# Performance work log

Measured on AMD Instinct MI355X. Metric: run time of the kernel, lower is better.

Reference implementation:

```python
import jax, jax.numpy as jnp
import numpy as np

B, O, D = 4096, 256, 256  # batch, size_out (rules), size_in (features)


def setup_inputs() -> dict:
    key = jax.random.key(0)
    k1, k2, k3, k4, k5 = jax.random.split(key, 5)
    return {
        "x": jax.random.normal(k1, (B, D), dtype=jnp.float32),
        "scales": jax.random.normal(k2, (O, D), dtype=jnp.float32),
        # strict upper triangle holds the packed rot vectors (original inits them to zeros;
        # small values keep the quadratic form well conditioned)
        "rots": jax.random.normal(k3, (O, D, D), dtype=jnp.float32) * 0.02,
        "centroids": jax.random.normal(k4, (O, D, 1), dtype=jnp.float32),
        "b": jax.random.uniform(k5, (O,), dtype=jnp.float32, minval=0.5, maxval=1.5),
    }


def reference(x, scales, rots, centroids, b):
    # Build symmetric transform A[o] = diag(scales[o]) + triu(rots[o],1) + triu(rots[o],1)^T
    # (equivalent to the loop of diag_embed(r_i, i+1) + mirrored lower diagonal).
    upper = jnp.triu(rots, 1)                                   # [O,D,D]
    A = upper + jnp.swapaxes(upper, -1, -2)
    A = A + jnp.eye(D, dtype=scales.dtype) * scales[:, None, :]  # diag_embed(scales)
    # Augmented affine map: mul[o,i,b'] = A[o] @ x[b'] + centroid[o,i]; const row dropped
    # since only the first size_in rows feed the norm.
    y = jnp.einsum('bj,oij->boi', x, A) + centroids[..., 0][None, :, :]  # [B,O,D]
    rx = jnp.sqrt(jnp.sum(y * y, axis=-1))                      # L2 norm over D -> [B,O]
    return 1.0 / (1.0 + rx ** (2.0 * b))                        # bell membership [B,O]
```

## Files before the change

kernel.cpp:

```cpp
#include <hip/hip_runtime.h>
#include <cstdint>
#include <cmath>

#define Bn 4096
#define Dn 256
#define On 256

typedef __bf16 v8bf __attribute__((ext_vector_type(8)));
typedef float  v4f  __attribute__((ext_vector_type(4)));
typedef unsigned short us8 __attribute__((ext_vector_type(8)));

__device__ __forceinline__ unsigned short f2bf(float f) {
    unsigned int u = __builtin_bit_cast(unsigned int, f);
    unsigned int r = (u + 0x7fffu + ((u >> 16) & 1u)) >> 16;
    return (unsigned short)r;
}

__device__ __forceinline__ void gl_lds16(const void* g, void* l) {
    __builtin_amdgcn_global_load_lds(
        (const __attribute__((address_space(1))) void*)(uintptr_t)g,
        (__attribute__((address_space(3))) void*)(uintptr_t)l, 16, 0, 0);
}

__global__ __launch_bounds__(256) void prep(
    const float* __restrict__ scales, const float* __restrict__ rots,
    const float* __restrict__ x, unsigned short* __restrict__ Ap,
    unsigned short* __restrict__ xb) {
    const int bid = blockIdx.x;
    const int tid = threadIdx.x;

    if (bid >= 2560) {
        const int cb = bid - 2560;
#pragma unroll
        for (int s = 0; s < 4; ++s) {
            const int i = cb * 4096 + s * 1024 + tid * 4;
            const float4 v = *(const float4*)(x + i);
            ushort4 u;
            u.x = f2bf(v.x); u.y = f2bf(v.y); u.z = f2bf(v.z); u.w = f2bf(v.w);
            *(ushort4*)(xb + i) = u;
        }
        return;
    }

    static const int TI[10] = {0, 0, 0, 0, 1, 1, 1, 2, 2, 3};
    static const int TJ[10] = {0, 1, 2, 3, 1, 2, 3, 2, 3, 3};
    const int o  = bid / 10;
    const int p  = bid - o * 10;
    const int ti = TI[p], tj = TJ[p];

    __shared__ float t[64][68];
    const float* src = rots + (size_t)o * Dn * Dn + (size_t)(ti * 64) * Dn + tj * 64;
#pragma unroll
    for (int s = 0; s < 4; ++s) {
        const int idx = s * 256 + tid;
        const int r = idx >> 4, c = (idx & 15) * 4;
        const float4 v = *(const float4*)(src + r * Dn + c);
        *(float4*)&t[r][c] = v;
    }
    __syncthreads();

#pragma unroll
    for (int it = 0; it < 2; ++it) {
        const int slot = it * 256 + tid;
        const int bk = slot >> 6, L = slot & 63;
        const int quad = L >> 4, frow = L & 15;
        const int sl = bk >> 1, kl = bk & 1;
        const int r = sl * 16 + frow, c = kl * 32 + quad * 8;
        float v[8];
        if (ti == tj) {
#pragma unroll
            for (int q = 0; q < 8; ++q) {
                const int cc = c + q;
                v[q] = (r < cc) ? t[r][cc]
                     : ((r > cc) ? t[cc][r] : scales[o * Dn + ti * 64 + r]);
            }
        } else {
            const float4 a = *(const float4*)&t[r][c];
            const float4 b = *(const float4*)&t[r][c + 4];
            v[0] = a.x; v[1] = a.y; v[2] = a.z; v[3] = a.w;
            v[4] = b.x; v[5] = b.y; v[6] = b.z; v[7] = b.w;
        }
        us8 u;
#pragma unroll
        for (int q = 0; q < 8; ++q) u[q] = f2bf(v[q]);
        const size_t off = ((size_t)((o * 16 + ti * 4 + sl) * 8 + tj * 2 + kl)) * 512 + L * 8;
        *(us8*)(Ap + off) = u;
    }

    if (ti != tj) {
#pragma unroll
        for (int it = 0; it < 2; ++it) {
            const int slot = it * 256 + tid;
            const int bk = slot >> 6, L = slot & 63;
            const int quad = L >> 4, frow = L & 15;
            const int sl = bk >> 1, kl = bk & 1;
            const int r = sl * 16 + frow, c = kl * 32 + quad * 8;
            us8 u;
#pragma unroll
            for (int q = 0; q < 8; ++q) u[q] = f2bf(t[c + q][r]);
            const size_t off = ((size_t)((o * 16 + tj * 4 + sl) * 8 + ti * 2 + kl)) * 512 + L * 8;
            *(us8*)(Ap + off) = u;
        }
    }
}

__global__ __launch_bounds__(256, 2) void fuzzy_main(
    const unsigned short* __restrict__ Ap, const unsigned short* __restrict__ xb,
    const float* __restrict__ cent, const float* __restrict__ bvals,
    float* __restrict__ obase, int sb, int so) {
    __shared__ __align__(16) unsigned short Xs[128 * 256];
    __shared__ float ssbuf[4][128];
    __shared__ float centL[Dn];

    const int tid  = threadIdx.x;
    const int lane = tid & 63;
    const int wv   = tid >> 6;
    const int Lb = blockIdx.x;
    const int o  = (Lb & 7) * 32 + (Lb >> 8);
    const int b0 = ((Lb >> 3) & 31) * 128;

    centL[tid] = cent[o * Dn + tid];

#pragma unroll
    for (int q = 0; q < 16; ++q) {
        const int R   = wv * 16 + q;
        const int row = 2 * R + (lane >> 5);
        const int g   = (lane & 31) ^ (row & 7);
        gl_lds16(xb + (size_t)(b0 + row) * Dn + g * 8, &Xs[R * 512 + lane * 8]);
    }
    __syncthreads();

    const int frow = lane & 15, quad = lane >> 4, f3 = lane & 7;
    const unsigned short* Aw = Ap + (size_t)(o * 16 + wv * 4) * 4096;

    v4f acc[4][8];
#pragma unroll
    for (int mi = 0; mi < 4; ++mi)
#pragma unroll
        for (int ni = 0; ni < 8; ++ni)
            acc[mi][ni] = v4f{0.f, 0.f, 0.f, 0.f};

    v8bf af[2][4];
#pragma unroll
    for (int mi = 0; mi < 4; ++mi)
        af[0][mi] = *(const v8bf*)(Aw + (size_t)mi * 8 * 512 + lane * 8);

#pragma unroll
    for (int t = 0; t < 8; ++t) {
        const int cur = t & 1, nxt = cur ^ 1;
        if (t < 7) {
#pragma unroll
            for (int mi = 0; mi < 4; ++mi)
                af[nxt][mi] = *(const v8bf*)(Aw + (size_t)(mi * 8 + t + 1) * 512 + lane * 8);
        }
        v8bf xf[8];
        const int sl = (t * 4 + quad) ^ f3;
#pragma unroll
        for (int ni = 0; ni < 8; ++ni)
            xf[ni] = *(const v8bf*)&Xs[(ni * 16 + frow) * 256 + sl * 8];
#pragma unroll
        for (int mi = 0; mi < 4; ++mi)
#pragma unroll
            for (int ni = 0; ni < 8; ++ni)
                acc[mi][ni] = __builtin_amdgcn_mfma_f32_16x16x32_bf16(
                    af[cur][mi], xf[ni], acc[mi][ni], 0, 0, 0);
    }

    float cv[4][4];
#pragma unroll
    for (int mi = 0; mi < 4; ++mi)
#pragma unroll
        for (int rg = 0; rg < 4; ++rg)
            cv[mi][rg] = centL[wv * 64 + mi * 16 + quad * 4 + rg];
#pragma unroll
    for (int ni = 0; ni < 8; ++ni) {
        float v = 0.f;
#pragma unroll
        for (int mi = 0; mi < 4; ++mi)
#pragma unroll
            for (int rg = 0; rg < 4; ++rg) {
                const float y = acc[mi][ni][rg] + cv[mi][rg];
                v += y * y;
            }
        v += __shfl_xor(v, 16);
        v += __shfl_xor(v, 32);
        if (lane < 16) ssbuf[wv][ni * 16 + lane] = v;
    }
    __syncthreads();
    if (tid < 128) {
        const float ssq = ssbuf[0][tid] + ssbuf[1][tid] + ssbuf[2][tid] + ssbuf[3][tid];
        obase[(size_t)(b0 + tid) * sb + (size_t)o * so] =
            1.0f / (1.0f + powf(ssq, bvals[o]));
    }
}

__global__ __launch_bounds__(256) void transp(const float* __restrict__ outT,
                                              float* __restrict__ out) {
    __shared__ float t[64][65];
    const int bb = blockIdx.x * 64;
    const int ob = blockIdx.y * 64;
    const int tid = threadIdx.x;
    const int r = tid >> 4;
    const int c = (tid & 15) * 4;
#pragma unroll
    for (int s = 0; s < 4; ++s) {
        const int rr = s * 16 + r;
        const float4 v = *(const float4*)(outT + (size_t)(ob + rr) * Bn + bb + c);
        t[rr][c] = v.x; t[rr][c + 1] = v.y; t[rr][c + 2] = v.z; t[rr][c + 3] = v.w;
    }
    __syncthreads();
#pragma unroll
    for (int s = 0; s < 4; ++s) {
        const int rr = s * 16 + r;
        float4 w;
        w.x = t[c][rr]; w.y = t[c + 1][rr]; w.z = t[c + 2][rr]; w.w = t[c + 3][rr];
        *(float4*)(out + (size_t)(bb + rr) * On + ob + c) = w;
    }
}

__global__ void fallback_kernel(const float* __restrict__ x, const float* __restrict__ scales,
                                const float* __restrict__ rots, const float* __restrict__ cent,
                                const float* __restrict__ bvals, float* __restrict__ out) {
    const int b = blockIdx.x * blockDim.x + threadIdx.x;
    const int o = blockIdx.y;
    if (b >= Bn) return;
    const float* R  = rots + (size_t)o * Dn * Dn;
    const float* xv = x + (size_t)b * Dn;
    float ss = 0.f;
    for (int i = 0; i < Dn; ++i) {
        float a = cent[o * Dn + i];
        for (int j = 0; j < Dn; ++j) {
            const float w = (j > i) ? R[i * Dn + j]
                          : ((j < i) ? R[j * Dn + i] : scales[o * Dn + i]);
            a += w * xv[j];
        }
        ss += a * a;
    }
    out[(size_t)b * On + o] = 1.f / (1.f + powf(ss, bvals[o]));
}

extern "C" void kernel_launch(void* const* d_in, const int* in_sizes, int n_in,
                              void* d_out, int out_size, void* d_ws, size_t ws_size,
                              hipStream_t stream) {
    const float* x         = (const float*)d_in[0];
    const float* scales    = (const float*)d_in[1];
    const float* rots      = (const float*)d_in[2];
    const float* centroids = (const float*)d_in[3];
    const float* bvals     = (const float*)d_in[4];
    float* out = (float*)d_out;

    const size_t needA = (size_t)On * Dn * Dn * sizeof(unsigned short);
    const size_t needX = (size_t)Bn * Dn * sizeof(unsigned short);
    const size_t needT = (size_t)On * Bn * sizeof(float);

    if (ws_size >= needA + needX) {
        unsigned short* Ap = (unsigned short*)d_ws;
        unsigned short* xb = (unsigned short*)((char*)d_ws + needA);
        prep<<<dim3(2816), 256, 0, stream>>>(scales, rots, x, Ap, xb);
        if (ws_size >= needA + needX + needT) {
            float* outT = (float*)((char*)d_ws + needA + needX);
            fuzzy_main<<<dim3(8192), 256, 0, stream>>>(Ap, xb, centroids, bvals,
                                                       outT, 1, Bn);
            transp<<<dim3(Bn / 64, On / 64), 256, 0, stream>>>(outT, out);
        } else {
            fuzzy_main<<<dim3(8192), 256, 0, stream>>>(Ap, xb, centroids, bvals,
                                                       out, On, 1);
        }
    } else {
        fallback_kernel<<<dim3(Bn / 256, On), 256, 0, stream>>>(x, scales, rots, centroids,
                                                                bvals, out);
    }
}
```

Baseline: 249.4 us.

## Process four rules per block to reuse X tile and drop transpose kernel

```diff
diff --git a/kernel.cpp b/kernel.cpp
--- a/kernel.cpp
+++ b/kernel.cpp
@@ -107,114 +107,105 @@
 __global__ __launch_bounds__(256, 2) void fuzzy_main(
     const unsigned short* __restrict__ Ap, const unsigned short* __restrict__ xb,
     const float* __restrict__ cent, const float* __restrict__ bvals,
-    float* __restrict__ obase, int sb, int so) {
-    __shared__ __align__(16) unsigned short Xs[128 * 256];
-    __shared__ float ssbuf[4][128];
-    __shared__ float centL[Dn];
+    float* __restrict__ out) {
+    __shared__ __align__(16) unsigned short Xs[4][128 * 64];
+    __shared__ float ssbufA[4][4][128];
+    __shared__ float centL[4][Dn];
 
     const int tid  = threadIdx.x;
     const int lane = tid & 63;
     const int wv   = tid >> 6;
     const int Lb = blockIdx.x;
-    const int o  = (Lb & 7) * 32 + (Lb >> 8);
+    const int og = (Lb & 7) * 8 + (Lb >> 8);
     const int b0 = ((Lb >> 3) & 31) * 128;
 
-    centL[tid] = cent[o * Dn + tid];
-
-#pragma unroll
-    for (int q = 0; q < 16; ++q) {
-        const int R   = wv * 16 + q;
-        const int row = 2 * R + (lane >> 5);
-        const int g   = (lane & 31) ^ (row & 7);
-        gl_lds16(xb + (size_t)(b0 + row) * Dn + g * 8, &Xs[R * 512 + lane * 8]);
-    }
+#pragma unroll
+    for (int op = 0; op < 4; ++op)
+        centL[op][tid] = cent[(og * 4 + op) * Dn + tid];
+
+    const int frow = lane & 15, quad = lane >> 4, f3 = lane & 7;
+    const int lr = lane >> 3, ls = lane & 7;
+    const int ksw = (ls ^ lr) * 8;
+
+#pragma unroll
+    for (int c = 0; c < 4; ++c)
+#pragma unroll
+        for (int q = 0; q < 4; ++q) {
+            const int row = (wv * 4 + q) * 8 + lr;
+            gl_lds16(xb + (size_t)(b0 + row) * Dn + c * 64 + ksw,
+                     &Xs[c][row * 64 + ls * 8]);
+        }
     __syncthreads();
 
-    const int frow = lane & 15, quad = lane >> 4, f3 = lane & 7;
-    const unsigned short* Aw = Ap + (size_t)(o * 16 + wv * 4) * 4096;
-
-    v4f acc[4][8];
-#pragma unroll
-    for (int mi = 0; mi < 4; ++mi)
-#pragma unroll
-        for (int ni = 0; ni < 8; ++ni)
-            acc[mi][ni] = v4f{0.f, 0.f, 0.f, 0.f};
-
-    v8bf af[2][4];
-#pragma unroll
-    for (int mi = 0; mi < 4; ++mi)
-        af[0][mi] = *(const v8bf*)(Aw + (size_t)mi * 8 * 512 + lane * 8);
-
-#pragma unroll
-    for (int t = 0; t < 8; ++t) {
-        const int cur = t & 1, nxt = cur ^ 1;
-        if (t < 7) {
+    for (int op = 0; op < 4; ++op) {
+        const int o = og * 4 + op;
+        const unsigned short* Aw = Ap + (size_t)(o * 16 + wv * 4) * 4096;
+
+        v4f acc[4][8];
+#pragma unroll
+        for (int mi = 0; mi < 4; ++mi)
+#pragma unroll
+            for (int ni = 0; ni < 8; ++ni)
+                acc[mi][ni] = v4f{0.f, 0.f, 0.f, 0.f};
+
+        v8bf af[2][4];
+#pragma unroll
+        for (int mi = 0; mi < 4; ++mi)
+            af[0][mi] = *(const v8bf*)(Aw + (size_t)mi * 8 * 512 + lane * 8);
+
+#pragma unroll
+        for (int t = 0; t < 8; ++t) {
+            const int cur = t & 1, nxt = cur ^ 1;
+            if (t < 7) {
+#pragma unroll
+                for (int mi = 0; mi < 4; ++mi)
+                    af[nxt][mi] = *(const v8bf*)(Aw + (size_t)(mi * 8 + t + 1) * 512 + lane * 8);
+            }
+            v8bf xf[8];
+            const int sl = ((t & 1) * 4 + quad) ^ f3;
+#pragma unroll
+            for (int ni = 0; ni < 8; ++ni)
+                xf[ni] = *(const v8bf*)&Xs[t >> 1][(ni * 16 + frow) * 64 + sl * 8];
 #pragma unroll
             for (int mi = 0; mi < 4; ++mi)
-                af[nxt][mi] = *(const v8bf*)(Aw + (size_t)(mi * 8 + t + 1) * 512 + lane * 8);
-        }
-        v8bf xf[8];
-        const int sl = (t * 4 + quad) ^ f3;
-#pragma unroll
-        for (int ni = 0; ni < 8; ++ni)
-            xf[ni] = *(const v8bf*)&Xs[(ni * 16 + frow) * 256 + sl * 8];
+#pragma unroll
+                for (int ni = 0; ni < 8; ++ni)
+                    acc[mi][ni] = __builtin_amdgcn_mfma_f32_16x16x32_bf16(
+                        af[cur][mi], xf[ni], acc[mi][ni], 0, 0, 0);
+        }
+
+        float cv[4][4];
 #pragma unroll
         for (int mi = 0; mi < 4; ++mi)
 #pragma unroll
-            for (int ni = 0; ni < 8; ++ni)
-                acc[mi][ni] = __builtin_amdgcn_mfma_f32_16x16x32_bf16(
-                    af[cur][mi], xf[ni], acc[mi][ni], 0, 0, 0);
-    }
-
-    float cv[4][4];
-#pragma unroll
-    for (int mi = 0; mi < 4; ++mi)
-#pragma unroll
-        for (int rg = 0; rg < 4; ++rg)
-            cv[mi][rg] = centL[wv * 64 + mi * 16 + quad * 4 + rg];
-#pragma unroll
-    for (int ni = 0; ni < 8; ++ni) {
-        float v = 0.f;
-#pragma unroll
-        for (int mi = 0; mi < 4; ++mi)
-#pragma unroll
-            for (int rg = 0; rg < 4; ++rg) {
-                const float y = acc[mi][ni][rg] + cv[mi][rg];
-                v += y * y;
-            }
-        v += __shfl_xor(v, 16);
-        v += __shfl_xor(v, 32);
-        if (lane < 16) ssbuf[wv][ni * 16 + lane] = v;
+            for (int rg = 0; rg < 4; ++rg)
+                cv[mi][rg] = centL[op][wv * 64 + mi * 16 + quad * 4 + rg];
+#pragma unroll
+        for (int ni = 0; ni < 8; ++ni) {
+            float v = 0.f;
+#pragma unroll
+            for (int mi = 0; mi < 4; ++mi)
+#pragma unroll
+                for (int rg = 0; rg < 4; ++rg) {
+                    const float y = acc[mi][ni][rg] + cv[mi][rg];
+                    v += y * y;
+                }
+            v += __shfl_xor(v, 16);
+            v += __shfl_xor(v, 32);
+            if (lane < 16) ssbufA[op][wv][ni * 16 + lane] = v;
+        }
     }
     __syncthreads();
     if (tid < 128) {
-        const float ssq = ssbuf[0][tid] + ssbuf[1][tid] + ssbuf[2][tid] + ssbuf[3][tid];
-        obase[(size_t)(b0 + tid) * sb + (size_t)o * so] =
-            1.0f / (1.0f + powf(ssq, bvals[o]));
-    }
-}
-
-__global__ __launch_bounds__(256) void transp(const float* __restrict__ outT,
-                                              float* __restrict__ out) {
-    __shared__ float t[64][65];
-    const int bb = blockIdx.x * 64;
-    const int ob = blockIdx.y * 64;
-    const int tid = threadIdx.x;
-    const int r = tid >> 4;
-    const int c = (tid & 15) * 4;
-#pragma unroll
-    for (int s = 0; s < 4; ++s) {
-        const int rr = s * 16 + r;
-        const float4 v = *(const float4*)(outT + (size_t)(ob + rr) * Bn + bb + c);
-        t[rr][c] = v.x; t[rr][c + 1] = v.y; t[rr][c + 2] = v.z; t[rr][c + 3] = v.w;
-    }
-    __syncthreads();
-#pragma unroll
-    for (int s = 0; s < 4; ++s) {
-        const int rr = s * 16 + r;
-        float4 w;
-        w.x = t[c][rr]; w.y = t[c + 1][rr]; w.z = t[c + 2][rr]; w.w = t[c + 3][rr];
-        *(float4*)(out + (size_t)(bb + rr) * On + ob + c) = w;
+        float4 r;
+        float* rp = &r.x;
+#pragma unroll
+        for (int op = 0; op < 4; ++op) {
+            const float ssq = ssbufA[op][0][tid] + ssbufA[op][1][tid] +
+                              ssbufA[op][2][tid] + ssbufA[op][3][tid];
+            rp[op] = 1.0f / (1.0f + powf(ssq, bvals[og * 4 + op]));
+        }
+        *(float4*)(out + (size_t)(b0 + tid) * On + og * 4) = r;
     }
 }
 
@@ -251,21 +242,12 @@
 
     const size_t needA = (size_t)On * Dn * Dn * sizeof(unsigned short);
     const size_t needX = (size_t)Bn * Dn * sizeof(unsigned short);
-    const size_t needT = (size_t)On * Bn * sizeof(float);
 
     if (ws_size >= needA + needX) {
         unsigned short* Ap = (unsigned short*)d_ws;
         unsigned short* xb = (unsigned short*)((char*)d_ws + needA);
         prep<<<dim3(2816), 256, 0, stream>>>(scales, rots, x, Ap, xb);
-        if (ws_size >= needA + needX + needT) {
-            float* outT = (float*)((char*)d_ws + needA + needX);
-            fuzzy_main<<<dim3(8192), 256, 0, stream>>>(Ap, xb, centroids, bvals,
-                                                       outT, 1, Bn);
-            transp<<<dim3(Bn / 64, On / 64), 256, 0, stream>>>(outT, out);
-        } else {
-            fuzzy_main<<<dim3(8192), 256, 0, stream>>>(Ap, xb, centroids, bvals,
-                                                       out, On, 1);
-        }
+        fuzzy_main<<<dim3(2048), 256, 0, stream>>>(Ap, xb, centroids, bvals, out);
     } else {
         fallback_kernel<<<dim3(Bn / 256, On), 256, 0, stream>>>(x, scales, rots, centroids,
                                                                 bvals, out);
```

After: 487.3 us. 1.95x slower.

## Switch main GEMM to 32x32x16 bf16 MFMA with matching operand layouts

Applied to the files above, without the earlier changes.

```diff
diff --git a/kernel.cpp b/kernel.cpp
--- a/kernel.cpp
+++ b/kernel.cpp
@@ -7,7 +7,7 @@
 #define On 256
 
 typedef __bf16 v8bf __attribute__((ext_vector_type(8)));
-typedef float  v4f  __attribute__((ext_vector_type(4)));
+typedef float  v16f __attribute__((ext_vector_type(16)));
 typedef unsigned short us8 __attribute__((ext_vector_type(8)));
 
 __device__ __forceinline__ unsigned short f2bf(float f) {
@@ -59,46 +59,43 @@
     }
     __syncthreads();
 
+    const int L   = tid & 63;
+    const int kl  = (tid >> 6) & 3;
+    const int i32 = L & 31;
+    const int kb  = kl * 16 + (L >> 5) * 8;
+
 #pragma unroll
     for (int it = 0; it < 2; ++it) {
-        const int slot = it * 256 + tid;
-        const int bk = slot >> 6, L = slot & 63;
-        const int quad = L >> 4, frow = L & 15;
-        const int sl = bk >> 1, kl = bk & 1;
-        const int r = sl * 16 + frow, c = kl * 32 + quad * 8;
+        const int r = it * 32 + i32;
         float v[8];
         if (ti == tj) {
 #pragma unroll
             for (int q = 0; q < 8; ++q) {
-                const int cc = c + q;
+                const int cc = kb + q;
                 v[q] = (r < cc) ? t[r][cc]
                      : ((r > cc) ? t[cc][r] : scales[o * Dn + ti * 64 + r]);
             }
         } else {
-            const float4 a = *(const float4*)&t[r][c];
-            const float4 b = *(const float4*)&t[r][c + 4];
+            const float4 a = *(const float4*)&t[r][kb];
+            const float4 b = *(const float4*)&t[r][kb + 4];
             v[0] = a.x; v[1] = a.y; v[2] = a.z; v[3] = a.w;
             v[4] = b.x; v[5] = b.y; v[6] = b.z; v[7] = b.w;
         }
         us8 u;
 #pragma unroll
         for (int q = 0; q < 8; ++q) u[q] = f2bf(v[q]);
-        const size_t off = ((size_t)((o * 16 + ti * 4 + sl) * 8 + tj * 2 + kl)) * 512 + L * 8;
+        const size_t off = ((size_t)((o * 8 + ti * 2 + it) * 16 + tj * 4 + kl)) * 512 + L * 8;
         *(us8*)(Ap + off) = u;
     }
 
     if (ti != tj) {
 #pragma unroll
         for (int it = 0; it < 2; ++it) {
-            const int slot = it * 256 + tid;
-            const int bk = slot >> 6, L = slot & 63;
-            const int quad = L >> 4, frow = L & 15;
-            const int sl = bk >> 1, kl = bk & 1;
-            const int r = sl * 16 + frow, c = kl * 32 + quad * 8;
+            const int r = it * 32 + i32;
             us8 u;
 #pragma unroll
-            for (int q = 0; q < 8; ++q) u[q] = f2bf(t[c + q][r]);
-            const size_t off = ((size_t)((o * 16 + tj * 4 + sl) * 8 + ti * 2 + kl)) * 512 + L * 8;
+            for (int q = 0; q < 8; ++q) u[q] = f2bf(t[kb + q][r]);
+            const size_t off = ((size_t)((o * 8 + tj * 2 + it) * 16 + ti * 4 + kl)) * 512 + L * 8;
             *(us8*)(Ap + off) = u;
         }
     }
@@ -108,7 +105,7 @@
     const unsigned short* __restrict__ Ap, const unsigned short* __restrict__ xb,
     const float* __restrict__ cent, const float* __restrict__ bvals,
     float* __restrict__ obase, int sb, int so) {
-    __shared__ __align__(16) unsigned short Xs[128 * 256];
+    __shared__ __align__(16) unsigned short Xs[64 * 512];
     __shared__ float ssbuf[4][128];
     __shared__ float centL[Dn];
 
@@ -123,68 +120,67 @@
 
 #pragma unroll
     for (int q = 0; q < 16; ++q) {
-        const int R   = wv * 16 + q;
-        const int row = 2 * R + (lane >> 5);
-        const int g   = (lane & 31) ^ (row & 7);
-        gl_lds16(xb + (size_t)(b0 + row) * Dn + g * 8, &Xs[R * 512 + lane * 8]);
-    }
-    __syncthreads();
-
-    const int frow = lane & 15, quad = lane >> 4, f3 = lane & 7;
-    const unsigned short* Aw = Ap + (size_t)(o * 16 + wv * 4) * 4096;
-
-    v4f acc[4][8];
-#pragma unroll
-    for (int mi = 0; mi < 4; ++mi)
-#pragma unroll
-        for (int ni = 0; ni < 8; ++ni)
-            acc[mi][ni] = v4f{0.f, 0.f, 0.f, 0.f};
-
-    v8bf af[2][4];
-#pragma unroll
-    for (int mi = 0; mi < 4; ++mi)
-        af[0][mi] = *(const v8bf*)(Aw + (size_t)mi * 8 * 512 + lane * 8);
-
-#pragma unroll
-    for (int t = 0; t < 8; ++t) {
+        const int R  = wv * 16 + q;
+        const int tt = R >> 2, nb = R & 3;
+        gl_lds16(xb + (size_t)(b0 + nb * 32 + (lane & 31)) * Dn + tt * 16 + (lane >> 5) * 8,
+                 &Xs[R * 512 + lane * 8]);
+    }
+
+    const unsigned short* Aw = Ap + (size_t)(o * 8 + wv * 2) * 16 * 512;
+
+    v16f acc[2][4];
+#pragma unroll
+    for (int mi = 0; mi < 2; ++mi)
+#pragma unroll
+        for (int nb = 0; nb < 4; ++nb)
+#pragma unroll
+            for (int rg = 0; rg < 16; ++rg)
+                acc[mi][nb][rg] = 0.f;
+
+    v8bf af[2][2], xf[2][4];
+#pragma unroll
+    for (int mi = 0; mi < 2; ++mi)
+        af[0][mi] = *(const v8bf*)(Aw + (size_t)(mi * 16) * 512 + lane * 8);
+
+    __syncthreads();
+
+#pragma unroll
+    for (int nb = 0; nb < 4; ++nb)
+        xf[0][nb] = *(const v8bf*)&Xs[nb * 512 + lane * 8];
+
+#pragma unroll
+    for (int t = 0; t < 16; ++t) {
         const int cur = t & 1, nxt = cur ^ 1;
-        if (t < 7) {
-#pragma unroll
-            for (int mi = 0; mi < 4; ++mi)
-                af[nxt][mi] = *(const v8bf*)(Aw + (size_t)(mi * 8 + t + 1) * 512 + lane * 8);
-        }
-        v8bf xf[8];
-        const int sl = (t * 4 + quad) ^ f3;
-#pragma unroll
-        for (int ni = 0; ni < 8; ++ni)
-            xf[ni] = *(const v8bf*)&Xs[(ni * 16 + frow) * 256 + sl * 8];
-#pragma unroll
-        for (int mi = 0; mi < 4; ++mi)
-#pragma unroll
-            for (int ni = 0; ni < 8; ++ni)
-                acc[mi][ni] = __builtin_amdgcn_mfma_f32_16x16x32_bf16(
-                    af[cur][mi], xf[ni], acc[mi][ni], 0, 0, 0);
-    }
-
-    float cv[4][4];
-#pragma unroll
-    for (int mi = 0; mi < 4; ++mi)
-#pragma unroll
-        for (int rg = 0; rg < 4; ++rg)
-            cv[mi][rg] = centL[wv * 64 + mi * 16 + quad * 4 + rg];
-#pragma unroll
-    for (int ni = 0; ni < 8; ++ni) {
+        if (t < 15) {
+#pragma unroll
+            for (int mi = 0; mi < 2; ++mi)
+                af[nxt][mi] = *(const v8bf*)(Aw + (size_t)(mi * 16 + t + 1) * 512 + lane * 8);
+#pragma unroll
+            for (int nb = 0; nb < 4; ++nb)
+                xf[nxt][nb] = *(const v8bf*)&Xs[((t + 1) * 4 + nb) * 512 + lane * 8];
+        }
+#pragma unroll
+        for (int mi = 0; mi < 2; ++mi)
+#pragma unroll
+            for (int nb = 0; nb < 4; ++nb)
+                acc[mi][nb] = __builtin_amdgcn_mfma_f32_32x32x16_bf16(
+                    af[cur][mi], xf[cur][nb], acc[mi][nb], 0, 0, 0);
+    }
+
+    const int half = lane >> 5;
+#pragma unroll
+    for (int nb = 0; nb < 4; ++nb) {
         float v = 0.f;
 #pragma unroll
-        for (int mi = 0; mi < 4; ++mi)
-#pragma unroll
-            for (int rg = 0; rg < 4; ++rg) {
-                const float y = acc[mi][ni][rg] + cv[mi][rg];
+        for (int mi = 0; mi < 2; ++mi)
+#pragma unroll
+            for (int rg = 0; rg < 16; ++rg) {
+                const int io = (rg & 3) + 8 * (rg >> 2) + 4 * half;
+                const float y = acc[mi][nb][rg] + centL[wv * 64 + mi * 32 + io];
                 v += y * y;
             }
-        v += __shfl_xor(v, 16);
         v += __shfl_xor(v, 32);
-        if (lane < 16) ssbuf[wv][ni * 16 + lane] = v;
+        if (lane < 32) ssbuf[wv][nb * 32 + lane] = v;
     }
     __syncthreads();
     if (tid < 128) {
```

New measurement: 275.3 us. 10.4% more time.
